# Kernel optimization log

Measured on AMD Instinct MI355X. Metric: run time of the kernel, lower is better.

Reference implementation:

```python
import jax, jax.numpy as jnp
import numpy as np

LAMBDA_C = 1.0
LAMBDA_S = 1.0
MARGIN = 0.05
HUBER_DELTA = 0.1
COS_EPS = 1e-8


def setup_inputs() -> dict:
    key = jax.random.key(0)
    k1, k2, k3, k4 = jax.random.split(key, 4)
    B, D = 4096, 2048
    return {
        "z_ref": jax.random.normal(k1, (B, D), dtype=jnp.float32),
        "z_perf": jax.random.normal(k2, (B, D), dtype=jnp.float32),
        "predicted_scores": jax.random.uniform(k3, (B, 4), dtype=jnp.float32),
        "target_scores": jax.random.uniform(k4, (B, 5), dtype=jnp.float32),
    }


def _cosine_sim(a, b):
    # torch.F.cosine_similarity with eps=1e-8: clamp each norm from below
    na = jnp.maximum(jnp.linalg.norm(a, axis=-1), COS_EPS)
    nb = jnp.maximum(jnp.linalg.norm(b, axis=-1), COS_EPS)
    return jnp.sum(a * b, axis=-1) / (na * nb)


def _contrastive(z_ref, z_perf, target_scores):
    sim = _cosine_sim(z_ref, z_perf)            # [B]
    overall = target_scores[:, 4]               # [B]
    # ordered pairs (i, j) with overall[i] > overall[j] contribute
    # relu(sim[j] - sim[i] + margin); each unordered pair fires at most once.
    mask = overall[:, None] > overall[None, :]                     # [B, B]
    pair_loss = jax.nn.relu(sim[None, :] - sim[:, None] + MARGIN)  # [B, B]
    n_pairs = jnp.sum(mask).astype(sim.dtype)
    total = jnp.sum(jnp.where(mask, pair_loss, jnp.zeros_like(pair_loss)))
    return jnp.where(n_pairs > 0, total / jnp.maximum(n_pairs, 1.0), 0.0)


def _huber(pred, tgt, delta):
    d = pred - tgt
    ad = jnp.abs(d)
    per = jnp.where(ad <= delta, 0.5 * d * d, delta * (ad - 0.5 * delta))
    return jnp.mean(per)


def reference(z_ref, z_perf, predicted_scores, target_scores):
    L_c = _contrastive(z_ref, z_perf, target_scores)
    L_s = _huber(predicted_scores, target_scores[:, :4], HUBER_DELTA)
    total = LAMBDA_C * L_c + LAMBDA_S * L_s
    return (total, L_c, L_s)
```

## Files before the change

kernel.cpp:

```cpp
#include <hip/hip_runtime.h>
#include <math.h>

#define B_ROWS 4096
#define D_DIM  2048
#define PAIR_BLOCKS 1024
#define ROWS_PER_PAIR_BLOCK (B_ROWS / PAIR_BLOCKS)
#define MARGIN_F 0.05f
#define HUBER_DELTA_F 0.1f
#define COS_EPS_F 1e-8f

__global__ __launch_bounds__(256) void sim_huber_kernel(
    const float* __restrict__ z_ref, const float* __restrict__ z_perf,
    const float* __restrict__ pred, const float* __restrict__ tgt,
    float* __restrict__ sim, float* __restrict__ overall,
    float* __restrict__ hub_part)
{
    const int row = blockIdx.x;
    const int tid = threadIdx.x;
    const float4* a4 = (const float4*)(z_ref + (size_t)row * D_DIM);
    const float4* b4 = (const float4*)(z_perf + (size_t)row * D_DIM);

    float dot = 0.f, na2 = 0.f, nb2 = 0.f;
    #pragma unroll
    for (int k = 0; k < 2; ++k) {
        const int idx = tid + k * 256;
        float4 a = a4[idx];
        float4 b = b4[idx];
        dot += a.x*b.x + a.y*b.y + a.z*b.z + a.w*b.w;
        na2 += a.x*a.x + a.y*a.y + a.z*a.z + a.w*a.w;
        nb2 += b.x*b.x + b.y*b.y + b.z*b.z + b.w*b.w;
    }

    __shared__ float hs[4];
    if (tid < 4) {
        float d  = pred[row * 4 + tid] - tgt[row * 5 + tid];
        float ad = fabsf(d);
        hs[tid] = (ad <= HUBER_DELTA_F) ? 0.5f * d * d
                                        : HUBER_DELTA_F * (ad - 0.5f * HUBER_DELTA_F);
    }

    const int lane = tid & 63, wave = tid >> 6;
    #pragma unroll
    for (int off = 32; off > 0; off >>= 1) {
        dot += __shfl_down(dot, off, 64);
        na2 += __shfl_down(na2, off, 64);
        nb2 += __shfl_down(nb2, off, 64);
    }
    __shared__ float shm[3][4];
    if (lane == 0) { shm[0][wave] = dot; shm[1][wave] = na2; shm[2][wave] = nb2; }
    __syncthreads();
    if (tid == 0) {
        float dt = shm[0][0] + shm[0][1] + shm[0][2] + shm[0][3];
        float na = sqrtf(shm[1][0] + shm[1][1] + shm[1][2] + shm[1][3]);
        float nb = sqrtf(shm[2][0] + shm[2][1] + shm[2][2] + shm[2][3]);
        na = fmaxf(na, COS_EPS_F);
        nb = fmaxf(nb, COS_EPS_F);
        sim[row] = dt / (na * nb);
        overall[row] = tgt[row * 5 + 4];
        hub_part[row] = hs[0] + hs[1] + hs[2] + hs[3];
    }
}

__global__ __launch_bounds__(256) void pair_kernel(
    const float* __restrict__ sim, const float* __restrict__ overall,
    float* __restrict__ pair_part, unsigned int* __restrict__ cnt_part)
{
    __shared__ float ls[B_ROWS];
    __shared__ float lo[B_ROWS];
    const int tid = threadIdx.x;

    const float4* s4 = (const float4*)sim;
    const float4* o4 = (const float4*)overall;
    float4* ls4 = (float4*)ls;
    float4* lo4 = (float4*)lo;
    #pragma unroll
    for (int k = 0; k < (B_ROWS / 4) / 256; ++k) {
        const int idx = tid + k * 256;
        ls4[idx] = s4[idx];
        lo4[idx] = o4[idx];
    }
    __syncthreads();

    const int i0 = blockIdx.x * ROWS_PER_PAIR_BLOCK;
    float s_i[ROWS_PER_PAIR_BLOCK], o_i[ROWS_PER_PAIR_BLOCK];
    #pragma unroll
    for (int ii = 0; ii < ROWS_PER_PAIR_BLOCK; ++ii) {
        s_i[ii] = ls[i0 + ii];
        o_i[ii] = lo[i0 + ii];
    }

    float part = 0.f;
    unsigned int cnt = 0;
    for (int j = tid; j < B_ROWS; j += 256) {
        float sj = ls[j];
        float oj = lo[j];
        #pragma unroll
        for (int ii = 0; ii < ROWS_PER_PAIR_BLOCK; ++ii) {
            if (o_i[ii] > oj) {
                part += fmaxf(sj - s_i[ii] + MARGIN_F, 0.f);
                cnt++;
            }
        }
    }

    const int lane = tid & 63, wave = tid >> 6;
    #pragma unroll
    for (int off = 32; off > 0; off >>= 1) {
        part += __shfl_down(part, off, 64);
        cnt  += __shfl_down(cnt,  off, 64);
    }
    __shared__ float pw[4];
    __shared__ unsigned int cw[4];
    if (lane == 0) { pw[wave] = part; cw[wave] = cnt; }
    __syncthreads();
    if (tid == 0) {
        pair_part[blockIdx.x] = pw[0] + pw[1] + pw[2] + pw[3];
        cnt_part[blockIdx.x]  = cw[0] + cw[1] + cw[2] + cw[3];
    }
}

__global__ __launch_bounds__(256) void finalize_kernel(
    const float* __restrict__ hub_part, const float* __restrict__ pair_part,
    const unsigned int* __restrict__ cnt_part, float* __restrict__ out)
{
    const int tid = threadIdx.x;
    float hub = 0.f, pr = 0.f;
    unsigned int cnt = 0;
    for (int k = tid; k < B_ROWS; k += 256) hub += hub_part[k];
    for (int k = tid; k < PAIR_BLOCKS; k += 256) {
        pr  += pair_part[k];
        cnt += cnt_part[k];
    }

    const int lane = tid & 63, wave = tid >> 6;
    #pragma unroll
    for (int off = 32; off > 0; off >>= 1) {
        hub += __shfl_down(hub, off, 64);
        pr  += __shfl_down(pr,  off, 64);
        cnt += __shfl_down(cnt, off, 64);
    }
    __shared__ float hw[4], pw[4];
    __shared__ unsigned int cw[4];
    if (lane == 0) { hw[wave] = hub; pw[wave] = pr; cw[wave] = cnt; }
    __syncthreads();
    if (tid == 0) {
        float H = hw[0] + hw[1] + hw[2] + hw[3];
        float P = pw[0] + pw[1] + pw[2] + pw[3];
        unsigned int C = cw[0] + cw[1] + cw[2] + cw[3];
        float n   = (float)C;
        float L_c = (n > 0.f) ? P / fmaxf(n, 1.f) : 0.f;
        float L_s = H / (float)(B_ROWS * 4);
        out[0] = L_c + L_s;
        out[1] = L_c;
        out[2] = L_s;
    }
}

extern "C" void kernel_launch(void* const* d_in, const int* in_sizes, int n_in,
                              void* d_out, int out_size, void* d_ws, size_t ws_size,
                              hipStream_t stream) {
    const float* z_ref  = (const float*)d_in[0];
    const float* z_perf = (const float*)d_in[1];
    const float* pred   = (const float*)d_in[2];
    const float* tgt    = (const float*)d_in[3];
    float* out = (float*)d_out;

    float* ws        = (float*)d_ws;
    float* sim       = ws;
    float* overall   = ws + B_ROWS;
    float* hub_part  = ws + 2 * B_ROWS;
    float* pair_part = ws + 3 * B_ROWS;
    unsigned int* cnt_part = (unsigned int*)(ws + 3 * B_ROWS + PAIR_BLOCKS);

    sim_huber_kernel<<<B_ROWS, 256, 0, stream>>>(z_ref, z_perf, pred, tgt,
                                                 sim, overall, hub_part);
    pair_kernel<<<PAIR_BLOCKS, 256, 0, stream>>>(sim, overall, pair_part, cnt_part);
    finalize_kernel<<<1, 256, 0, stream>>>(hub_part, pair_part, cnt_part, out);
}
```

Baseline: 106.1 us.

## Fuse three kernels into one cooperative kernel with grid syncs

Merges the similarity/Huber, pair-loss and finalize kernels into one cooperative launch of 1024 blocks, separated by grid-wide syncs. Each wave now computes one row's cosine similarity. The pair stage reads sim/overall straight from global memory, with no LDS staging. The aim is to remove two launch boundaries and the per-block shared-memory copy. In exchange it adds two grid barriers and relies on all 1024 blocks being co-resident (256 CUs × 4 blocks).

New measurement: 323.6 us. +204.9%, slower.

```diff
diff --git a/kernel.cpp b/kernel.cpp
--- a/kernel.cpp
+++ b/kernel.cpp
@@ -1,158 +1,139 @@
 #include <hip/hip_runtime.h>
+#include <hip/hip_cooperative_groups.h>
 #include <math.h>
+
+namespace cg = cooperative_groups;
 
 #define B_ROWS 4096
 #define D_DIM  2048
-#define PAIR_BLOCKS 1024
-#define ROWS_PER_PAIR_BLOCK (B_ROWS / PAIR_BLOCKS)
+#define NBLK   1024
+#define ROWS_PER_BLK (B_ROWS / NBLK)
 #define MARGIN_F 0.05f
 #define HUBER_DELTA_F 0.1f
 #define COS_EPS_F 1e-8f
 
-__global__ __launch_bounds__(256) void sim_huber_kernel(
+__global__ __launch_bounds__(256, 4) void fused_kernel(
     const float* __restrict__ z_ref, const float* __restrict__ z_perf,
     const float* __restrict__ pred, const float* __restrict__ tgt,
     float* __restrict__ sim, float* __restrict__ overall,
-    float* __restrict__ hub_part)
+    float* __restrict__ pair_part, float* __restrict__ hub_part,
+    unsigned int* __restrict__ cnt_part, float* __restrict__ out)
 {
-    const int row = blockIdx.x;
-    const int tid = threadIdx.x;
-    const float4* a4 = (const float4*)(z_ref + (size_t)row * D_DIM);
-    const float4* b4 = (const float4*)(z_perf + (size_t)row * D_DIM);
+    __shared__ float hubw[4];
+    __shared__ float pw[4];
+    __shared__ float hw[4];
+    __shared__ unsigned int cw[4];
 
-    float dot = 0.f, na2 = 0.f, nb2 = 0.f;
-    #pragma unroll
-    for (int k = 0; k < 2; ++k) {
-        const int idx = tid + k * 256;
-        float4 a = a4[idx];
-        float4 b = b4[idx];
-        dot += a.x*b.x + a.y*b.y + a.z*b.z + a.w*b.w;
-        na2 += a.x*a.x + a.y*a.y + a.z*a.z + a.w*a.w;
-        nb2 += b.x*b.x + b.y*b.y + b.z*b.z + b.w*b.w;
-    }
+    const int tid  = threadIdx.x;
+    const int lane = tid & 63;
+    const int wave = tid >> 6;
+    const int bid  = blockIdx.x;
 
-    __shared__ float hs[4];
-    if (tid < 4) {
-        float d  = pred[row * 4 + tid] - tgt[row * 5 + tid];
-        float ad = fabsf(d);
-        hs[tid] = (ad <= HUBER_DELTA_F) ? 0.5f * d * d
+    {
+        const int row = bid * ROWS_PER_BLK + wave;
+        const float4* a4 = (const float4*)(z_ref + (size_t)row * D_DIM);
+        const float4* b4 = (const float4*)(z_perf + (size_t)row * D_DIM);
+        float dot = 0.f, na2 = 0.f, nb2 = 0.f;
+        #pragma unroll
+        for (int k = 0; k < 8; ++k) {
+            float4 a = a4[lane + k * 64];
+            float4 b = b4[lane + k * 64];
+            dot += a.x*b.x + a.y*b.y + a.z*b.z + a.w*b.w;
+            na2 += a.x*a.x + a.y*a.y + a.z*a.z + a.w*a.w;
+            nb2 += b.x*b.x + b.y*b.y + b.z*b.z + b.w*b.w;
+        }
+        #pragma unroll
+        for (int off = 32; off > 0; off >>= 1) {
+            dot += __shfl_down(dot, off, 64);
+            na2 += __shfl_down(na2, off, 64);
+            nb2 += __shfl_down(nb2, off, 64);
+        }
+        float hub = 0.f;
+        if (lane < 4) {
+            float d  = pred[row * 4 + lane] - tgt[row * 5 + lane];
+            float ad = fabsf(d);
+            hub = (ad <= HUBER_DELTA_F) ? 0.5f * d * d
                                         : HUBER_DELTA_F * (ad - 0.5f * HUBER_DELTA_F);
-    }
-
-    const int lane = tid & 63, wave = tid >> 6;
-    #pragma unroll
-    for (int off = 32; off > 0; off >>= 1) {
-        dot += __shfl_down(dot, off, 64);
-        na2 += __shfl_down(na2, off, 64);
-        nb2 += __shfl_down(nb2, off, 64);
-    }
-    __shared__ float shm[3][4];
-    if (lane == 0) { shm[0][wave] = dot; shm[1][wave] = na2; shm[2][wave] = nb2; }
-    __syncthreads();
-    if (tid == 0) {
-        float dt = shm[0][0] + shm[0][1] + shm[0][2] + shm[0][3];
-        float na = sqrtf(shm[1][0] + shm[1][1] + shm[1][2] + shm[1][3]);
-        float nb = sqrtf(shm[2][0] + shm[2][1] + shm[2][2] + shm[2][3]);
-        na = fmaxf(na, COS_EPS_F);
-        nb = fmaxf(nb, COS_EPS_F);
-        sim[row] = dt / (na * nb);
-        overall[row] = tgt[row * 5 + 4];
-        hub_part[row] = hs[0] + hs[1] + hs[2] + hs[3];
-    }
-}
-
-__global__ __launch_bounds__(256) void pair_kernel(
-    const float* __restrict__ sim, const float* __restrict__ overall,
-    float* __restrict__ pair_part, unsigned int* __restrict__ cnt_part)
-{
-    __shared__ float ls[B_ROWS];
-    __shared__ float lo[B_ROWS];
-    const int tid = threadIdx.x;
-
-    const float4* s4 = (const float4*)sim;
-    const float4* o4 = (const float4*)overall;
-    float4* ls4 = (float4*)ls;
-    float4* lo4 = (float4*)lo;
-    #pragma unroll
-    for (int k = 0; k < (B_ROWS / 4) / 256; ++k) {
-        const int idx = tid + k * 256;
-        ls4[idx] = s4[idx];
-        lo4[idx] = o4[idx];
-    }
-    __syncthreads();
-
-    const int i0 = blockIdx.x * ROWS_PER_PAIR_BLOCK;
-    float s_i[ROWS_PER_PAIR_BLOCK], o_i[ROWS_PER_PAIR_BLOCK];
-    #pragma unroll
-    for (int ii = 0; ii < ROWS_PER_PAIR_BLOCK; ++ii) {
-        s_i[ii] = ls[i0 + ii];
-        o_i[ii] = lo[i0 + ii];
-    }
-
-    float part = 0.f;
-    unsigned int cnt = 0;
-    for (int j = tid; j < B_ROWS; j += 256) {
-        float sj = ls[j];
-        float oj = lo[j];
-        #pragma unroll
-        for (int ii = 0; ii < ROWS_PER_PAIR_BLOCK; ++ii) {
-            if (o_i[ii] > oj) {
-                part += fmaxf(sj - s_i[ii] + MARGIN_F, 0.f);
-                cnt++;
-            }
+        }
+        hub += __shfl_down(hub, 2, 64);
+        hub += __shfl_down(hub, 1, 64);
+        if (lane == 0) {
+            float na = fmaxf(sqrtf(na2), COS_EPS_F);
+            float nb = fmaxf(sqrtf(nb2), COS_EPS_F);
+            sim[row]     = dot / (na * nb);
+            overall[row] = tgt[row * 5 + 4];
+            hubw[wave]   = hub;
         }
     }
 
-    const int lane = tid & 63, wave = tid >> 6;
-    #pragma unroll
-    for (int off = 32; off > 0; off >>= 1) {
-        part += __shfl_down(part, off, 64);
-        cnt  += __shfl_down(cnt,  off, 64);
-    }
-    __shared__ float pw[4];
-    __shared__ unsigned int cw[4];
-    if (lane == 0) { pw[wave] = part; cw[wave] = cnt; }
-    __syncthreads();
-    if (tid == 0) {
-        pair_part[blockIdx.x] = pw[0] + pw[1] + pw[2] + pw[3];
-        cnt_part[blockIdx.x]  = cw[0] + cw[1] + cw[2] + cw[3];
-    }
-}
+    cg::this_grid().sync();
 
-__global__ __launch_bounds__(256) void finalize_kernel(
-    const float* __restrict__ hub_part, const float* __restrict__ pair_part,
-    const unsigned int* __restrict__ cnt_part, float* __restrict__ out)
-{
-    const int tid = threadIdx.x;
-    float hub = 0.f, pr = 0.f;
-    unsigned int cnt = 0;
-    for (int k = tid; k < B_ROWS; k += 256) hub += hub_part[k];
-    for (int k = tid; k < PAIR_BLOCKS; k += 256) {
-        pr  += pair_part[k];
-        cnt += cnt_part[k];
+    {
+        const int i0 = bid * ROWS_PER_BLK;
+        float s_i[ROWS_PER_BLK], o_i[ROWS_PER_BLK];
+        #pragma unroll
+        for (int ii = 0; ii < ROWS_PER_BLK; ++ii) {
+            s_i[ii] = sim[i0 + ii];
+            o_i[ii] = overall[i0 + ii];
+        }
+        float part = 0.f;
+        unsigned int cnt = 0;
+        #pragma unroll 4
+        for (int j = tid; j < B_ROWS; j += 256) {
+            float sj = sim[j];
+            float oj = overall[j];
+            #pragma unroll
+            for (int ii = 0; ii < ROWS_PER_BLK; ++ii) {
+                if (o_i[ii] > oj) {
+                    part += fmaxf(sj - s_i[ii] + MARGIN_F, 0.f);
+                    cnt++;
+                }
+            }
+        }
+        #pragma unroll
+        for (int off = 32; off > 0; off >>= 1) {
+            part += __shfl_down(part, off, 64);
+            cnt  += __shfl_down(cnt,  off, 64);
+        }
+        if (lane == 0) { pw[wave] = part; cw[wave] = cnt; }
+        __syncthreads();
+        if (tid == 0) {
+            pair_part[bid] = pw[0] + pw[1] + pw[2] + pw[3];
+            cnt_part[bid]  = cw[0] + cw[1] + cw[2] + cw[3];
+            hub_part[bid]  = hubw[0] + hubw[1] + hubw[2] + hubw[3];
+        }
     }
 
-    const int lane = tid & 63, wave = tid >> 6;
-    #pragma unroll
-    for (int off = 32; off > 0; off >>= 1) {
-        hub += __shfl_down(hub, off, 64);
-        pr  += __shfl_down(pr,  off, 64);
-        cnt += __shfl_down(cnt, off, 64);
-    }
-    __shared__ float hw[4], pw[4];
-    __shared__ unsigned int cw[4];
-    if (lane == 0) { hw[wave] = hub; pw[wave] = pr; cw[wave] = cnt; }
-    __syncthreads();
-    if (tid == 0) {
-        float H = hw[0] + hw[1] + hw[2] + hw[3];
-        float P = pw[0] + pw[1] + pw[2] + pw[3];
-        unsigned int C = cw[0] + cw[1] + cw[2] + cw[3];
-        float n   = (float)C;
-        float L_c = (n > 0.f) ? P / fmaxf(n, 1.f) : 0.f;
-        float L_s = H / (float)(B_ROWS * 4);
-        out[0] = L_c + L_s;
-        out[1] = L_c;
-        out[2] = L_s;
+    cg::this_grid().sync();
+
+    if (bid == 0) {
+        float pr = 0.f, hb = 0.f;
+        unsigned int cnt = 0;
+        #pragma unroll
+        for (int k = tid; k < NBLK; k += 256) {
+            pr  += pair_part[k];
+            hb  += hub_part[k];
+            cnt += cnt_part[k];
+        }
+        #pragma unroll
+        for (int off = 32; off > 0; off >>= 1) {
+            pr  += __shfl_down(pr,  off, 64);
+            hb  += __shfl_down(hb,  off, 64);
+            cnt += __shfl_down(cnt, off, 64);
+        }
+        if (lane == 0) { pw[wave] = pr; hw[wave] = hb; cw[wave] = cnt; }
+        __syncthreads();
+        if (tid == 0) {
+            float P = pw[0] + pw[1] + pw[2] + pw[3];
+            float H = hw[0] + hw[1] + hw[2] + hw[3];
+            unsigned int C = cw[0] + cw[1] + cw[2] + cw[3];
+            float n   = (float)C;
+            float L_c = (n > 0.f) ? P / fmaxf(n, 1.f) : 0.f;
+            float L_s = H / (float)(B_ROWS * 4);
+            out[0] = L_c + L_s;
+            out[1] = L_c;
+            out[2] = L_s;
+        }
     }
 }
 
@@ -168,12 +149,12 @@
     float* ws        = (float*)d_ws;
     float* sim       = ws;
     float* overall   = ws + B_ROWS;
-    float* hub_part  = ws + 2 * B_ROWS;
-    float* pair_part = ws + 3 * B_ROWS;
-    unsigned int* cnt_part = (unsigned int*)(ws + 3 * B_ROWS + PAIR_BLOCKS);
+    float* pair_part = ws + 2 * B_ROWS;
+    float* hub_part  = ws + 2 * B_ROWS + NBLK;
+    unsigned int* cnt_part = (unsigned int*)(ws + 2 * B_ROWS + 2 * NBLK);
 
-    sim_huber_kernel<<<B_ROWS, 256, 0, stream>>>(z_ref, z_perf, pred, tgt,
-                                                 sim, overall, hub_part);
-    pair_kernel<<<PAIR_BLOCKS, 256, 0, stream>>>(sim, overall, pair_part, cnt_part);
-    finalize_kernel<<<1, 256, 0, stream>>>(hub_part, pair_part, cnt_part, out);
+    void* args[] = { &z_ref, &z_perf, &pred, &tgt, &sim, &overall,
+                     &pair_part, &hub_part, &cnt_part, &out };
+    hipLaunchCooperativeKernel((const void*)fused_kernel, dim3(NBLK), dim3(256),
+                               args, 0, stream);
 }
```

## Cut pair kernel to 256 blocks of 16 rows and move Huber into it

Applied to the files above, without the earlier changes.

The pair kernel now runs 256 blocks that each handle 16 rows instead of 1024 blocks of 4 rows. This cuts the redundant per-block staging of sim and overall into shared memory from global memory by four times. The Huber term moves out of the similarity kernel into the pair kernel, one element per thread, and finalize now reads one partial per thread. The trade-off is fewer blocks to fill the GPU, with more serial compare work per thread and more registers.

Result: no change. 107.4 us (+1.2%).

```diff
diff --git a/kernel.cpp b/kernel.cpp
--- a/kernel.cpp
+++ b/kernel.cpp
@@ -3,17 +3,17 @@
 
 #define B_ROWS 4096
 #define D_DIM  2048
-#define PAIR_BLOCKS 1024
-#define ROWS_PER_PAIR_BLOCK (B_ROWS / PAIR_BLOCKS)
+#define NBLK_B 256
+#define ROWS_PER_B (B_ROWS / NBLK_B)
 #define MARGIN_F 0.05f
 #define HUBER_DELTA_F 0.1f
 #define COS_EPS_F 1e-8f
 
-__global__ __launch_bounds__(256) void sim_huber_kernel(
+
+__global__ __launch_bounds__(256) void sim_kernel(
     const float* __restrict__ z_ref, const float* __restrict__ z_perf,
-    const float* __restrict__ pred, const float* __restrict__ tgt,
-    float* __restrict__ sim, float* __restrict__ overall,
-    float* __restrict__ hub_part)
+    const float* __restrict__ tgt,
+    float* __restrict__ sim, float* __restrict__ overall)
 {
     const int row = blockIdx.x;
     const int tid = threadIdx.x;
@@ -31,14 +31,6 @@
         nb2 += b.x*b.x + b.y*b.y + b.z*b.z + b.w*b.w;
     }
 
-    __shared__ float hs[4];
-    if (tid < 4) {
-        float d  = pred[row * 4 + tid] - tgt[row * 5 + tid];
-        float ad = fabsf(d);
-        hs[tid] = (ad <= HUBER_DELTA_F) ? 0.5f * d * d
-                                        : HUBER_DELTA_F * (ad - 0.5f * HUBER_DELTA_F);
-    }
-
     const int lane = tid & 63, wave = tid >> 6;
     #pragma unroll
     for (int off = 32; off > 0; off >>= 1) {
@@ -51,22 +43,24 @@
     __syncthreads();
     if (tid == 0) {
         float dt = shm[0][0] + shm[0][1] + shm[0][2] + shm[0][3];
-        float na = sqrtf(shm[1][0] + shm[1][1] + shm[1][2] + shm[1][3]);
-        float nb = sqrtf(shm[2][0] + shm[2][1] + shm[2][2] + shm[2][3]);
-        na = fmaxf(na, COS_EPS_F);
-        nb = fmaxf(nb, COS_EPS_F);
-        sim[row] = dt / (na * nb);
+        float na = fmaxf(sqrtf(shm[1][0] + shm[1][1] + shm[1][2] + shm[1][3]), COS_EPS_F);
+        float nb = fmaxf(sqrtf(shm[2][0] + shm[2][1] + shm[2][2] + shm[2][3]), COS_EPS_F);
+        sim[row]     = dt / (na * nb);
         overall[row] = tgt[row * 5 + 4];
-        hub_part[row] = hs[0] + hs[1] + hs[2] + hs[3];
     }
 }
 
 __global__ __launch_bounds__(256) void pair_kernel(
     const float* __restrict__ sim, const float* __restrict__ overall,
-    float* __restrict__ pair_part, unsigned int* __restrict__ cnt_part)
+    const float* __restrict__ pred, const float* __restrict__ tgt,
+    float* __restrict__ pair_part, float* __restrict__ hub_part,
+    unsigned int* __restrict__ cnt_part)
 {
     __shared__ float ls[B_ROWS];
     __shared__ float lo[B_ROWS];
+    __shared__ float pw[4], hw[4];
+    __shared__ unsigned int cw[4];
+
     const int tid = threadIdx.x;
 
     const float4* s4 = (const float4*)sim;
@@ -79,12 +73,22 @@
         ls4[idx] = s4[idx];
         lo4[idx] = o4[idx];
     }
+
+    const int i0 = blockIdx.x * ROWS_PER_B;
+    float hub = 0.f;
+    if (tid < ROWS_PER_B * 4) {
+        const int r = i0 + (tid >> 2);
+        const int e = tid & 3;
+        float d  = pred[r * 4 + e] - tgt[r * 5 + e];
+        float ad = fabsf(d);
+        hub = (ad <= HUBER_DELTA_F) ? 0.5f * d * d
+                                    : HUBER_DELTA_F * (ad - 0.5f * HUBER_DELTA_F);
+    }
     __syncthreads();
 
-    const int i0 = blockIdx.x * ROWS_PER_PAIR_BLOCK;
-    float s_i[ROWS_PER_PAIR_BLOCK], o_i[ROWS_PER_PAIR_BLOCK];
+    float s_i[ROWS_PER_B], o_i[ROWS_PER_B];
     #pragma unroll
-    for (int ii = 0; ii < ROWS_PER_PAIR_BLOCK; ++ii) {
+    for (int ii = 0; ii < ROWS_PER_B; ++ii) {
         s_i[ii] = ls[i0 + ii];
         o_i[ii] = lo[i0 + ii];
     }
@@ -95,7 +99,7 @@
         float sj = ls[j];
         float oj = lo[j];
         #pragma unroll
-        for (int ii = 0; ii < ROWS_PER_PAIR_BLOCK; ++ii) {
+        for (int ii = 0; ii < ROWS_PER_B; ++ii) {
             if (o_i[ii] > oj) {
                 part += fmaxf(sj - s_i[ii] + MARGIN_F, 0.f);
                 cnt++;
@@ -108,14 +112,14 @@
     for (int off = 32; off > 0; off >>= 1) {
         part += __shfl_down(part, off, 64);
         cnt  += __shfl_down(cnt,  off, 64);
+        hub  += __shfl_down(hub,  off, 64);
     }
-    __shared__ float pw[4];
-    __shared__ unsigned int cw[4];
-    if (lane == 0) { pw[wave] = part; cw[wave] = cnt; }
+    if (lane == 0) { pw[wave] = part; cw[wave] = cnt; hw[wave] = hub; }
     __syncthreads();
     if (tid == 0) {
         pair_part[blockIdx.x] = pw[0] + pw[1] + pw[2] + pw[3];
         cnt_part[blockIdx.x]  = cw[0] + cw[1] + cw[2] + cw[3];
+        hub_part[blockIdx.x]  = hw[0] + hw[1] + hw[2] + hw[3];
     }
 }
 
@@ -124,13 +128,9 @@
     const unsigned int* __restrict__ cnt_part, float* __restrict__ out)
 {
     const int tid = threadIdx.x;
-    float hub = 0.f, pr = 0.f;
-    unsigned int cnt = 0;
-    for (int k = tid; k < B_ROWS; k += 256) hub += hub_part[k];
-    for (int k = tid; k < PAIR_BLOCKS; k += 256) {
-        pr  += pair_part[k];
-        cnt += cnt_part[k];
-    }
+    float hub = hub_part[tid];
+    float pr  = pair_part[tid];
+    unsigned int cnt = cnt_part[tid];
 
     const int lane = tid & 63, wave = tid >> 6;
     #pragma unroll
@@ -168,12 +168,12 @@
     float* ws        = (float*)d_ws;
     float* sim       = ws;
     float* overall   = ws + B_ROWS;
-    float* hub_part  = ws + 2 * B_ROWS;
-    float* pair_part = ws + 3 * B_ROWS;
-    unsigned int* cnt_part = (unsigned int*)(ws + 3 * B_ROWS + PAIR_BLOCKS);
+    float* pair_part = ws + 2 * B_ROWS;
+    float* hub_part  = ws + 2 * B_ROWS + NBLK_B;
+    unsigned int* cnt_part = (unsigned int*)(ws + 2 * B_ROWS + 2 * NBLK_B);
 
-    sim_huber_kernel<<<B_ROWS, 256, 0, stream>>>(z_ref, z_perf, pred, tgt,
-                                                 sim, overall, hub_part);
-    pair_kernel<<<PAIR_BLOCKS, 256, 0, stream>>>(sim, overall, pair_part, cnt_part);
+    sim_kernel<<<B_ROWS, 256, 0, stream>>>(z_ref, z_perf, tgt, sim, overall);
+    pair_kernel<<<NBLK_B, 256, 0, stream>>>(sim, overall, pred, tgt,
+                                            pair_part, hub_part, cnt_part);
     finalize_kernel<<<1, 256, 0, stream>>>(hub_part, pair_part, cnt_part, out);
 }
```
